# Optimization experiments

Measured on AMD Instinct MI355X. Metric: run time of the kernel, lower is better.

Reference implementation:

```python
import jax, jax.numpy as jnp
import numpy as np

B, D, H, O, E = 16384, 256, 256, 256, 32
N_ACTIVE = 22          # int(32 * 0.7) from BoltzmannGate
TEMP = float(np.e)     # Boltzmann temperature
EPS = 1e-8


def setup_inputs() -> dict:
    key = jax.random.key(0)
    ks = jax.random.split(key, 7)
    s = 0.02  # init scale for weights
    return {
        "x":  jax.random.normal(ks[0], (B, D), dtype=jnp.float32),
        "W1": jax.random.normal(ks[1], (E, H, D), dtype=jnp.float32) * s,  # [E, out=H, in=D] torch Linear layout
        "b1": jax.random.normal(ks[2], (E, H), dtype=jnp.float32) * s,
        "W2": jax.random.normal(ks[3], (E, O, H), dtype=jnp.float32) * s,
        "b2": jax.random.normal(ks[4], (E, O), dtype=jnp.float32) * s,
        "Wg": jax.random.normal(ks[5], (E, D), dtype=jnp.float32) * s,
        "bg": jax.random.normal(ks[6], (E,), dtype=jnp.float32) * s,
    }


def reference(x, W1, b1, W2, b2, Wg, bg):
    # Dense all-experts forward: [B, E, H] -> relu -> [B, E, O]
    h = jax.nn.relu(jnp.einsum('bd,ehd->beh', x, W1) + b1[None, :, :])
    expert_out = jnp.einsum('beh,eoh->beo', h, W2) + b2[None, :, :]

    # Boltzmann gate: softmax(scores / T), keep top-k probs, renormalize.
    scores = (x @ Wg.T + bg) / TEMP                      # [B, E]
    probs = jax.nn.softmax(scores, axis=-1)
    _, topk_idx = jax.lax.top_k(probs, N_ACTIVE)         # [B, N_ACTIVE]
    mask = jnp.zeros_like(probs).at[jnp.arange(B)[:, None], topk_idx].set(1.0)
    weights = probs * mask
    weights = weights / (jnp.sum(weights, axis=-1, keepdims=True) + EPS)

    # Weighted combine over experts: [B, O]
    return jnp.einsum('be,beo->bo', weights, expert_out)
```

## Files before the change

### kernel.cpp

```cpp
#include <hip/hip_runtime.h>
#include <hip/hip_bf16.h>


typedef __attribute__((ext_vector_type(8))) short bf16x8;
typedef __attribute__((ext_vector_type(4))) float f32x4;
typedef __attribute__((ext_vector_type(16))) float f32x16;

__device__ __forceinline__ unsigned short f2bf(float f) {
    unsigned u = __builtin_bit_cast(unsigned, f);
    u += 0x7FFFu + ((u >> 16) & 1u);
    return (unsigned short)(u >> 16);
}
__device__ __forceinline__ unsigned pack_bf16x2(float a, float b) {
    return (unsigned)f2bf(a) | ((unsigned)f2bf(b) << 16);
}

#define LX(r, ch) (((r) << 8) + ((((ch) ^ ((r) & 7))) << 3))

__global__ __launch_bounds__(256) void cvt_w(const float* __restrict__ W1,
                                             const float* __restrict__ W2,
                                             unsigned short* __restrict__ Wr) {
    int T = blockIdx.x * 256 + threadIdx.x;
    int lane = T & 63, ks = (T >> 6) & 15, e = (T >> 10) & 31;
    int cg = (T >> 15) & 7, m = (T >> 18) & 1;
    int l31 = lane & 31, hi = lane >> 5;
    const float* src = (m ? W2 : W1) +
                       ((long)e * 256 + cg * 32 + l31) * 256 + ks * 16 + hi * 8;
    float4 v0 = ((const float4*)src)[0], v1 = ((const float4*)src)[1];
    uint4 o;
    o.x = pack_bf16x2(v0.x, v0.y); o.y = pack_bf16x2(v0.z, v0.w);
    o.z = pack_bf16x2(v1.x, v1.y); o.w = pack_bf16x2(v1.z, v1.w);
    long U = (((long)(m * 8 + cg) * 33 + e) * 16 + ks) * 64 + lane;
    ((uint4*)Wr)[U] = o;
}

#define MFMA32(A, B, C) __builtin_amdgcn_mfma_f32_32x32x16_bf16(A, B, C, 0, 0, 0)

#define GSTEP(j, BUF) do {                                                     \
    bf16x8 a0 = ra[j], a1 = rb[j];                                             \
    ra[j] = *(const bf16x8*)(pla + ((j) & 3) * 512);                           \
    rb[j] = *(const bf16x8*)(plb + ((j) & 3) * 512);                           \
    bf16x8 b0 = cba[(j) & 3], b1 = cbb[(j) & 3];                               \
    cba[(j) & 3] = *(const bf16x8*)(&(BUF)[LX(l31,      ckn + ((j) + 4) * 2)]);\
    cbb[(j) & 3] = *(const bf16x8*)(&(BUF)[LX(32 + l31, ckn + ((j) + 4) * 2)]);\
    __builtin_amdgcn_s_setprio(1);                                             \
    acc00 = MFMA32(a0, b0, acc00);                                             \
    acc01 = MFMA32(a0, b1, acc01);                                             \
    acc10 = MFMA32(a1, b0, acc10);                                             \
    acc11 = MFMA32(a1, b1, acc11);                                             \
    __builtin_amdgcn_s_setprio(0);                                             \
    if (((j) & 3) == 3) { pla += 2048; plb += 2048; }                          \
} while (0)

#define EPI(ACC, CG, RG) do {                                                  \
    const int rr = (RG) * 32 + l31;                                            \
    const float gw = gws[rr * 33 + e];                                         \
    const int rbase = rr << 8, rsw = rr & 7;                                   \
    _Pragma("unroll")                                                          \
    for (int q = 0; q < 4; ++q) {                                              \
        float4 bv = *(const float4*)(bias1 + e * 256 +                         \
                                     (2 * g + (CG)) * 32 + q * 8 + hi * 4);    \
        float v0 = fmaxf(ACC[4 * q + 0] + bv.x, 0.f) * gw;                     \
        float v1 = fmaxf(ACC[4 * q + 1] + bv.y, 0.f) * gw;                     \
        float v2 = fmaxf(ACC[4 * q + 2] + bv.z, 0.f) * gw;                     \
        float v3 = fmaxf(ACC[4 * q + 3] + bv.w, 0.f) * gw;                     \
        uint2 pk;                                                              \
        pk.x = pack_bf16x2(v0, v1);                                            \
        pk.y = pack_bf16x2(v2, v3);                                            \
        int ch = (2 * g + (CG)) * 4 + q;                                       \
        *(uint2*)(&hw[rbase + ((ch ^ rsw) << 3) + hi * 4]) = pk;               \
    }                                                                          \
} while (0)

__global__ __launch_bounds__(512)
__attribute__((amdgpu_waves_per_eu(2, 2)))
void moe_kernel(
    const float* __restrict__ x,
    const unsigned short* __restrict__ Wr,
    const float* __restrict__ bias1,
    const float* __restrict__ b2,
    const float* __restrict__ Wg,
    const float* __restrict__ bg,
    float* __restrict__ out)
{
    __shared__ __align__(16) unsigned short x_s[64 * 256];
    __shared__ __align__(16) unsigned short h_s[2][64 * 256];
    __shared__ float gws[64 * 33];

    const int tid  = threadIdx.x;
    const int wv   = tid >> 6, lane = tid & 63;
    const int l31  = lane & 31, hi = lane >> 5;
    const int crew = wv >> 2;
    const int g    = wv & 3;
    const int row0 = blockIdx.x * 64;

#pragma unroll
    for (int c = 0; c < 4; ++c) {
        int chunk = tid + c * 512;
        int r = chunk >> 5, ch = chunk & 31;
        const float4* s = (const float4*)(x + (long)(row0 + r) * 256 + ch * 8);
        float4 v0 = s[0], v1 = s[1];
        uint4 o;
        o.x = pack_bf16x2(v0.x, v0.y); o.y = pack_bf16x2(v0.z, v0.w);
        o.z = pack_bf16x2(v1.x, v1.y); o.w = pack_bf16x2(v1.z, v1.w);
        *(uint4*)(&x_s[LX(r, ch)]) = o;
    }

    {
        const int e32 = lane & 31, half = lane >> 5;
        const float4* wg4 = (const float4*)(Wg + e32 * 256 + half * 128);
        float bgv = bg[e32];
        for (int i = 0; i < 8; ++i) {
            int lr = wv * 8 + i;
            const float4* xr4 = (const float4*)(x + (long)(row0 + lr) * 256 + half * 128);
            float acc = 0.f;
#pragma unroll
            for (int tt = 0; tt < 32; ++tt) {
                float4 w = wg4[tt], xv = xr4[tt];
                acc = fmaf(w.x, xv.x, acc); acc = fmaf(w.y, xv.y, acc);
                acc = fmaf(w.z, xv.z, acc); acc = fmaf(w.w, xv.w, acc);
            }
            acc += __shfl_xor(acc, 32);
            float score = (acc + bgv) / 2.71828182845904523f;

            float m = score;
#pragma unroll
            for (int d = 16; d >= 1; d >>= 1) m = fmaxf(m, __shfl_xor(m, d));
            float p_ = expf(score - m);
            float ps = p_;
#pragma unroll
            for (int d = 16; d >= 1; d >>= 1) ps += __shfl_xor(ps, d);
            float prob = p_ / ps;

            int rank = 0;
#pragma unroll
            for (int j = 0; j < 32; ++j) {
                float pj = __shfl(prob, j);
                rank += (pj > prob || (pj == prob && j < e32)) ? 1 : 0;
            }
            float kept = (rank < 22) ? prob : 0.f;
            float wsum = kept;
#pragma unroll
            for (int d = 16; d >= 1; d >>= 1) wsum += __shfl_xor(wsum, d);
            float weight = kept / (wsum + 1e-8f);

            if (half == 0) gws[lr * 33 + e32] = weight;
        }
    }

    __syncthreads();

    const unsigned short* wa =
        Wr + (long)(crew * 8 + 2 * g) * (33 * 16 * 512) + lane * 8;
    const unsigned short* wb =
        Wr + (long)(crew * 8 + 2 * g + 1) * (33 * 16 * 512) + lane * 8;
    bf16x8 ra[8], rb[8];
#pragma unroll
    for (int t = 0; t < 8; ++t) {
        ra[t] = *(const bf16x8*)(wa + t * 512);
        rb[t] = *(const bf16x8*)(wb + t * 512);
    }
    const unsigned short* pla = wa + 8 * 512;
    const unsigned short* plb = wb + 8 * 512;

    bf16x8 cba[4], cbb[4];

    f32x16 acc00, acc01, acc10, acc11;
#pragma unroll
    for (int i = 0; i < 16; ++i) {
        acc00[i] = 0.f; acc01[i] = 0.f; acc10[i] = 0.f; acc11[i] = 0.f;
    }
    if (crew == 1) {
        for (int ee = 0; ee < 32; ++ee) {
            float gv0 = gws[l31 * 33 + ee];
            float gv1 = gws[(32 + l31) * 33 + ee];
#pragma unroll
            for (int q = 0; q < 4; ++q) {
                float4 b0 = *(const float4*)(b2 + ee * 256 + (2 * g) * 32 + q * 8 + hi * 4);
                float4 b1 = *(const float4*)(b2 + ee * 256 + (2 * g + 1) * 32 + q * 8 + hi * 4);
                acc00[4 * q + 0] = fmaf(gv0, b0.x, acc00[4 * q + 0]);
                acc00[4 * q + 1] = fmaf(gv0, b0.y, acc00[4 * q + 1]);
                acc00[4 * q + 2] = fmaf(gv0, b0.z, acc00[4 * q + 2]);
                acc00[4 * q + 3] = fmaf(gv0, b0.w, acc00[4 * q + 3]);
                acc01[4 * q + 0] = fmaf(gv1, b0.x, acc01[4 * q + 0]);
                acc01[4 * q + 1] = fmaf(gv1, b0.y, acc01[4 * q + 1]);
                acc01[4 * q + 2] = fmaf(gv1, b0.z, acc01[4 * q + 2]);
                acc01[4 * q + 3] = fmaf(gv1, b0.w, acc01[4 * q + 3]);
                acc10[4 * q + 0] = fmaf(gv0, b1.x, acc10[4 * q + 0]);
                acc10[4 * q + 1] = fmaf(gv0, b1.y, acc10[4 * q + 1]);
                acc10[4 * q + 2] = fmaf(gv0, b1.z, acc10[4 * q + 2]);
                acc10[4 * q + 3] = fmaf(gv0, b1.w, acc10[4 * q + 3]);
                acc11[4 * q + 0] = fmaf(gv1, b1.x, acc11[4 * q + 0]);
                acc11[4 * q + 1] = fmaf(gv1, b1.y, acc11[4 * q + 1]);
                acc11[4 * q + 2] = fmaf(gv1, b1.z, acc11[4 * q + 2]);
                acc11[4 * q + 3] = fmaf(gv1, b1.w, acc11[4 * q + 3]);
            }
        }
    }

#pragma unroll 1
    for (int e = 0; e <= 32; ++e) {
        if (crew == 0) {
            if (e < 32) {
#pragma unroll
                for (int i = 0; i < 16; ++i) {
                    acc00[i] = 0.f; acc01[i] = 0.f; acc10[i] = 0.f; acc11[i] = 0.f;
                }
#pragma unroll
                for (int t = 0; t < 4; ++t) {
                    cba[t] = *(const bf16x8*)(&x_s[LX(l31,      t * 2 + hi)]);
                    cbb[t] = *(const bf16x8*)(&x_s[LX(32 + l31, t * 2 + hi)]);
                }
#pragma unroll 1
                for (int g8 = 0; g8 < 2; ++g8) {
                    const int ckn = g8 * 16 + hi;
                    GSTEP(0, x_s); GSTEP(1, x_s); GSTEP(2, x_s); GSTEP(3, x_s);
                    GSTEP(4, x_s); GSTEP(5, x_s); GSTEP(6, x_s); GSTEP(7, x_s);
                }
                unsigned short* hw = h_s[e & 1];
                EPI(acc00, 0, 0);
                EPI(acc01, 0, 1);
                EPI(acc10, 1, 0);
                EPI(acc11, 1, 1);
            }
        } else {
            if (e >= 1) {
                const unsigned short* hbr = h_s[(e + 1) & 1];
#pragma unroll
                for (int t = 0; t < 4; ++t) {
                    cba[t] = *(const bf16x8*)(&hbr[LX(l31,      t * 2 + hi)]);
                    cbb[t] = *(const bf16x8*)(&hbr[LX(32 + l31, t * 2 + hi)]);
                }
#pragma unroll 1
                for (int g8 = 0; g8 < 2; ++g8) {
                    const int ckn = g8 * 16 + hi;
                    GSTEP(0, hbr); GSTEP(1, hbr); GSTEP(2, hbr); GSTEP(3, hbr);
                    GSTEP(4, hbr); GSTEP(5, hbr); GSTEP(6, hbr); GSTEP(7, hbr);
                }
            }
        }

        asm volatile("s_waitcnt lgkmcnt(0)" ::: "memory");
        __builtin_amdgcn_s_barrier();
    }

    if (crew == 1) {
#pragma unroll
        for (int q = 0; q < 4; ++q) {
            f32x4 s00 = {acc00[4 * q + 0], acc00[4 * q + 1],
                         acc00[4 * q + 2], acc00[4 * q + 3]};
            f32x4 s01 = {acc01[4 * q + 0], acc01[4 * q + 1],
                         acc01[4 * q + 2], acc01[4 * q + 3]};
            f32x4 s10 = {acc10[4 * q + 0], acc10[4 * q + 1],
                         acc10[4 * q + 2], acc10[4 * q + 3]};
            f32x4 s11 = {acc11[4 * q + 0], acc11[4 * q + 1],
                         acc11[4 * q + 2], acc11[4 * q + 3]};
            *(f32x4*)(out + (long)(row0 + l31) * 256 +
                      (2 * g) * 32 + q * 8 + hi * 4) = s00;
            *(f32x4*)(out + (long)(row0 + 32 + l31) * 256 +
                      (2 * g) * 32 + q * 8 + hi * 4) = s01;
            *(f32x4*)(out + (long)(row0 + l31) * 256 +
                      (2 * g + 1) * 32 + q * 8 + hi * 4) = s10;
            *(f32x4*)(out + (long)(row0 + 32 + l31) * 256 +
                      (2 * g + 1) * 32 + q * 8 + hi * 4) = s11;
        }
    }
}

extern "C" void kernel_launch(void* const* d_in, const int* in_sizes, int n_in,
                              void* d_out, int out_size, void* d_ws, size_t ws_size,
                              hipStream_t stream) {
    (void)in_sizes; (void)n_in; (void)out_size; (void)ws_size;
    const float* x  = (const float*)d_in[0];
    const float* W1 = (const float*)d_in[1];
    const float* b1 = (const float*)d_in[2];
    const float* W2 = (const float*)d_in[3];
    const float* b2 = (const float*)d_in[4];
    const float* Wg = (const float*)d_in[5];
    const float* bg = (const float*)d_in[6];
    float* out = (float*)d_out;

    unsigned short* Wr = (unsigned short*)d_ws;

    cvt_w<<<2048, 256, 0, stream>>>(W1, W2, Wr);
    moe_kernel<<<256, 512, 0, stream>>>(x, Wr, b1, b2, Wg, bg, out);
}
```

Before: 272.0 us.

## Double waves per block, each computing one 32-column group instead of two

```diff
diff --git a/kernel.cpp b/kernel.cpp
--- a/kernel.cpp
+++ b/kernel.cpp
@@ -37,29 +37,25 @@
 #define MFMA32(A, B, C) __builtin_amdgcn_mfma_f32_32x32x16_bf16(A, B, C, 0, 0, 0)
 
 #define GSTEP(j, BUF) do {                                                     \
-    bf16x8 a0 = ra[j], a1 = rb[j];                                             \
-    ra[j] = *(const bf16x8*)(pla + ((j) & 3) * 512);                           \
-    rb[j] = *(const bf16x8*)(plb + ((j) & 3) * 512);                           \
-    bf16x8 b0 = cba[(j) & 3], b1 = cbb[(j) & 3];                               \
-    cba[(j) & 3] = *(const bf16x8*)(&(BUF)[LX(l31,      ckn + ((j) + 4) * 2)]);\
-    cbb[(j) & 3] = *(const bf16x8*)(&(BUF)[LX(32 + l31, ckn + ((j) + 4) * 2)]);\
+    bf16x8 a = ra[(j) & 3];                                                    \
+    ra[(j) & 3] = *(const bf16x8*)(pla + ((j) & 3) * 512);                     \
+    bf16x8 b0 = cba[(j) & 1], b1 = cbb[(j) & 1];                               \
+    cba[(j) & 1] = *(const bf16x8*)(&(BUF)[LX(l31,      (ckn + ((j) + 2) * 2) & 31)]); \
+    cbb[(j) & 1] = *(const bf16x8*)(&(BUF)[LX(32 + l31, (ckn + ((j) + 2) * 2) & 31)]); \
     __builtin_amdgcn_s_setprio(1);                                             \
-    acc00 = MFMA32(a0, b0, acc00);                                             \
-    acc01 = MFMA32(a0, b1, acc01);                                             \
-    acc10 = MFMA32(a1, b0, acc10);                                             \
-    acc11 = MFMA32(a1, b1, acc11);                                             \
+    acc0 = MFMA32(a, b0, acc0);                                                \
+    acc1 = MFMA32(a, b1, acc1);                                                \
     __builtin_amdgcn_s_setprio(0);                                             \
-    if (((j) & 3) == 3) { pla += 2048; plb += 2048; }                          \
+    if (((j) & 3) == 3) { pla += 2048; }                                       \
 } while (0)
 
-#define EPI(ACC, CG, RG) do {                                                  \
+#define EPI(ACC, RG) do {                                                      \
     const int rr = (RG) * 32 + l31;                                            \
     const float gw = gws[rr * 33 + e];                                         \
     const int rbase = rr << 8, rsw = rr & 7;                                   \
     _Pragma("unroll")                                                          \
     for (int q = 0; q < 4; ++q) {                                              \
-        float4 bv = *(const float4*)(bias1 + e * 256 +                         \
-                                     (2 * g + (CG)) * 32 + q * 8 + hi * 4);    \
+        float4 bv = *(const float4*)(bias1 + e * 256 + cg * 32 + q * 8 + hi * 4); \
         float v0 = fmaxf(ACC[4 * q + 0] + bv.x, 0.f) * gw;                     \
         float v1 = fmaxf(ACC[4 * q + 1] + bv.y, 0.f) * gw;                     \
         float v2 = fmaxf(ACC[4 * q + 2] + bv.z, 0.f) * gw;                     \
@@ -67,13 +63,13 @@
         uint2 pk;                                                              \
         pk.x = pack_bf16x2(v0, v1);                                            \
         pk.y = pack_bf16x2(v2, v3);                                            \
-        int ch = (2 * g + (CG)) * 4 + q;                                       \
+        int ch = cg * 4 + q;                                                   \
         *(uint2*)(&hw[rbase + ((ch ^ rsw) << 3) + hi * 4]) = pk;               \
     }                                                                          \
 } while (0)
 
-__global__ __launch_bounds__(512)
-__attribute__((amdgpu_waves_per_eu(2, 2)))
+__global__ __launch_bounds__(1024)
+__attribute__((amdgpu_waves_per_eu(4, 4)))
 void moe_kernel(
     const float* __restrict__ x,
     const unsigned short* __restrict__ Wr,
@@ -90,13 +86,13 @@
     const int tid  = threadIdx.x;
     const int wv   = tid >> 6, lane = tid & 63;
     const int l31  = lane & 31, hi = lane >> 5;
-    const int crew = wv >> 2;
-    const int g    = wv & 3;
+    const int crew = wv >> 3;
+    const int cg   = wv & 7;
     const int row0 = blockIdx.x * 64;
 
 #pragma unroll
-    for (int c = 0; c < 4; ++c) {
-        int chunk = tid + c * 512;
+    for (int c = 0; c < 2; ++c) {
+        int chunk = tid + c * 1024;
         int r = chunk >> 5, ch = chunk & 31;
         const float4* s = (const float4*)(x + (long)(row0 + r) * 256 + ch * 8);
         float4 v0 = s[0], v1 = s[1];
@@ -110,8 +106,8 @@
         const int e32 = lane & 31, half = lane >> 5;
         const float4* wg4 = (const float4*)(Wg + e32 * 256 + half * 128);
         float bgv = bg[e32];
-        for (int i = 0; i < 8; ++i) {
-            int lr = wv * 8 + i;
+        for (int i = 0; i < 4; ++i) {
+            int lr = wv * 4 + i;
             const float4* xr4 = (const float4*)(x + (long)(row0 + lr) * 256 + half * 128);
             float acc = 0.f;
 #pragma unroll
@@ -150,50 +146,33 @@
 
     __syncthreads();
 
-    const unsigned short* wa =
-        Wr + (long)(crew * 8 + 2 * g) * (33 * 16 * 512) + lane * 8;
-    const unsigned short* wb =
-        Wr + (long)(crew * 8 + 2 * g + 1) * (33 * 16 * 512) + lane * 8;
-    bf16x8 ra[8], rb[8];
-#pragma unroll
-    for (int t = 0; t < 8; ++t) {
-        ra[t] = *(const bf16x8*)(wa + t * 512);
-        rb[t] = *(const bf16x8*)(wb + t * 512);
-    }
-    const unsigned short* pla = wa + 8 * 512;
-    const unsigned short* plb = wb + 8 * 512;
-
-    bf16x8 cba[4], cbb[4];
-
-    f32x16 acc00, acc01, acc10, acc11;
-#pragma unroll
-    for (int i = 0; i < 16; ++i) {
-        acc00[i] = 0.f; acc01[i] = 0.f; acc10[i] = 0.f; acc11[i] = 0.f;
-    }
+    const unsigned short* ws =
+        Wr + (long)(crew * 8 + cg) * (33 * 16 * 512) + lane * 8;
+    bf16x8 ra[4];
+#pragma unroll
+    for (int t = 0; t < 4; ++t) ra[t] = *(const bf16x8*)(ws + t * 512);
+    const unsigned short* pla = ws + 4 * 512;
+
+    bf16x8 cba[2], cbb[2];
+
+    f32x16 acc0, acc1;
+#pragma unroll
+    for (int i = 0; i < 16; ++i) { acc0[i] = 0.f; acc1[i] = 0.f; }
     if (crew == 1) {
         for (int ee = 0; ee < 32; ++ee) {
             float gv0 = gws[l31 * 33 + ee];
             float gv1 = gws[(32 + l31) * 33 + ee];
 #pragma unroll
             for (int q = 0; q < 4; ++q) {
-                float4 b0 = *(const float4*)(b2 + ee * 256 + (2 * g) * 32 + q * 8 + hi * 4);
-                float4 b1 = *(const float4*)(b2 + ee * 256 + (2 * g + 1) * 32 + q * 8 + hi * 4);
-                acc00[4 * q + 0] = fmaf(gv0, b0.x, acc00[4 * q + 0]);
-                acc00[4 * q + 1] = fmaf(gv0, b0.y, acc00[4 * q + 1]);
-                acc00[4 * q + 2] = fmaf(gv0, b0.z, acc00[4 * q + 2]);
-                acc00[4 * q + 3] = fmaf(gv0, b0.w, acc00[4 * q + 3]);
-                acc01[4 * q + 0] = fmaf(gv1, b0.x, acc01[4 * q + 0]);
-                acc01[4 * q + 1] = fmaf(gv1, b0.y, acc01[4 * q + 1]);
-                acc01[4 * q + 2] = fmaf(gv1, b0.z, acc01[4 * q + 2]);
-                acc01[4 * q + 3] = fmaf(gv1, b0.w, acc01[4 * q + 3]);
-                acc10[4 * q + 0] = fmaf(gv0, b1.x, acc10[4 * q + 0]);
-                acc10[4 * q + 1] = fmaf(gv0, b1.y, acc10[4 * q + 1]);
-                acc10[4 * q + 2] = fmaf(gv0, b1.z, acc10[4 * q + 2]);
-                acc10[4 * q + 3] = fmaf(gv0, b1.w, acc10[4 * q + 3]);
-                acc11[4 * q + 0] = fmaf(gv1, b1.x, acc11[4 * q + 0]);
-                acc11[4 * q + 1] = fmaf(gv1, b1.y, acc11[4 * q + 1]);
-                acc11[4 * q + 2] = fmaf(gv1, b1.z, acc11[4 * q + 2]);
-                acc11[4 * q + 3] = fmaf(gv1, b1.w, acc11[4 * q + 3]);
+                float4 bb = *(const float4*)(b2 + ee * 256 + cg * 32 + q * 8 + hi * 4);
+                acc0[4 * q + 0] = fmaf(gv0, bb.x, acc0[4 * q + 0]);
+                acc0[4 * q + 1] = fmaf(gv0, bb.y, acc0[4 * q + 1]);
+                acc0[4 * q + 2] = fmaf(gv0, bb.z, acc0[4 * q + 2]);
+                acc0[4 * q + 3] = fmaf(gv0, bb.w, acc0[4 * q + 3]);
+                acc1[4 * q + 0] = fmaf(gv1, bb.x, acc1[4 * q + 0]);
+                acc1[4 * q + 1] = fmaf(gv1, bb.y, acc1[4 * q + 1]);
+                acc1[4 * q + 2] = fmaf(gv1, bb.z, acc1[4 * q + 2]);
+                acc1[4 * q + 3] = fmaf(gv1, bb.w, acc1[4 * q + 3]);
             }
         }
     }
@@ -203,11 +182,9 @@
         if (crew == 0) {
             if (e < 32) {
 #pragma unroll
-                for (int i = 0; i < 16; ++i) {
-                    acc00[i] = 0.f; acc01[i] = 0.f; acc10[i] = 0.f; acc11[i] = 0.f;
-                }
-#pragma unroll
-                for (int t = 0; t < 4; ++t) {
+                for (int i = 0; i < 16; ++i) { acc0[i] = 0.f; acc1[i] = 0.f; }
+#pragma unroll
+                for (int t = 0; t < 2; ++t) {
                     cba[t] = *(const bf16x8*)(&x_s[LX(l31,      t * 2 + hi)]);
                     cbb[t] = *(const bf16x8*)(&x_s[LX(32 + l31, t * 2 + hi)]);
                 }
@@ -218,16 +195,14 @@
                     GSTEP(4, x_s); GSTEP(5, x_s); GSTEP(6, x_s); GSTEP(7, x_s);
                 }
                 unsigned short* hw = h_s[e & 1];
-                EPI(acc00, 0, 0);
-                EPI(acc01, 0, 1);
-                EPI(acc10, 1, 0);
-                EPI(acc11, 1, 1);
+                EPI(acc0, 0);
+                EPI(acc1, 1);
             }
         } else {
             if (e >= 1) {
                 const unsigned short* hbr = h_s[(e + 1) & 1];
 #pragma unroll
-                for (int t = 0; t < 4; ++t) {
+                for (int t = 0; t < 2; ++t) {
                     cba[t] = *(const bf16x8*)(&hbr[LX(l31,      t * 2 + hi)]);
                     cbb[t] = *(const bf16x8*)(&hbr[LX(32 + l31, t * 2 + hi)]);
                 }
@@ -247,22 +222,14 @@
     if (crew == 1) {
 #pragma unroll
         for (int q = 0; q < 4; ++q) {
-            f32x4 s00 = {acc00[4 * q + 0], acc00[4 * q + 1],
-                         acc00[4 * q + 2], acc00[4 * q + 3]};
-            f32x4 s01 = {acc01[4 * q + 0], acc01[4 * q + 1],
-                         acc01[4 * q + 2], acc01[4 * q + 3]};
-            f32x4 s10 = {acc10[4 * q + 0], acc10[4 * q + 1],
-                         acc10[4 * q + 2], acc10[4 * q + 3]};
-            f32x4 s11 = {acc11[4 * q + 0], acc11[4 * q + 1],
-                         acc11[4 * q + 2], acc11[4 * q + 3]};
+            f32x4 s0 = {acc0[4 * q + 0], acc0[4 * q + 1],
+                        acc0[4 * q + 2], acc0[4 * q + 3]};
+            f32x4 s1 = {acc1[4 * q + 0], acc1[4 * q + 1],
+                        acc1[4 * q + 2], acc1[4 * q + 3]};
             *(f32x4*)(out + (long)(row0 + l31) * 256 +
-                      (2 * g) * 32 + q * 8 + hi * 4) = s00;
+                      cg * 32 + q * 8 + hi * 4) = s0;
             *(f32x4*)(out + (long)(row0 + 32 + l31) * 256 +
-                      (2 * g) * 32 + q * 8 + hi * 4) = s01;
-            *(f32x4*)(out + (long)(row0 + l31) * 256 +
-                      (2 * g + 1) * 32 + q * 8 + hi * 4) = s10;
-            *(f32x4*)(out + (long)(row0 + 32 + l31) * 256 +
-                      (2 * g + 1) * 32 + q * 8 + hi * 4) = s11;
+                      cg * 32 + q * 8 + hi * 4) = s1;
         }
     }
 }
@@ -283,5 +250,5 @@
     unsigned short* Wr = (unsigned short*)d_ws;
 
     cvt_w<<<2048, 256, 0, stream>>>(W1, W2, Wr);
-    moe_kernel<<<256, 512, 0, stream>>>(x, Wr, b1, b2, Wg, bg, out);
-}
+    moe_kernel<<<256, 1024, 0, stream>>>(x, Wr, b1, b2, Wg, bg, out);
+}
```

Result: slower. 300.1 us (+10.3%).
